# Kernel tuning notes

Hardware: AMD Instinct MI355X
Metric: run time of the kernel (lower is better)

The kernel has to match this reference:

```python
import jax, jax.numpy as jnp
import numpy as np

N_ITER = 5
NMF_EPS = 1e-20
IP_EPS = 1e-20

M, J, I, K = 2, 2000, 2049, 8  # channels == sources, frames, freq bins, NMF bases


def setup_inputs() -> dict:
    key = jax.random.key(0)
    k1, k2, k3 = jax.random.split(key, 3)
    X = jax.random.normal(k1, (M, J, I, 2), dtype=jnp.float32)
    lo = 1e-08
    T0 = jax.random.uniform(k2, (I, K, M), dtype=jnp.float32) * (1 - lo) + lo
    V0 = jax.random.uniform(k3, (K, J, M), dtype=jnp.float32) * (1 - lo) + lo
    return {"X": X, "T0": T0, "V0": V0}


def nmf_update(T, V, Y, eps):
    # T: (I,K), V: (K,J), Y: (I,J) complex
    P = jnp.abs(Y) ** 2                       # power spectrogram (I,J)
    R = T @ V                                  # low-rank model (I,J)
    T = T * jnp.sqrt(((P / (R * R)) @ V.T) / ((1.0 / R) @ V.T))
    T = jnp.maximum(T, eps)
    R = T @ V
    V = V * jnp.sqrt((T.T @ (P / (R * R))) / (T.T @ (1.0 / R)))
    V = jnp.maximum(V, eps)
    R = T @ V
    return T, V, R


def reference(X, T0, V0):
    Mc, Jc, Ic, _ = X.shape
    N = Mc
    # view_as_complex(X.permute(2,0,1,3)) -> (I, M, J) complex
    Xc = jnp.transpose(X[..., 0] + 1j * X[..., 1], (2, 0, 1)).astype(jnp.complex64)
    eye_M = jnp.eye(Mc, dtype=jnp.complex64)
    W = jnp.broadcast_to(eye_M, (Ic, N, Mc))   # (I, N, M)
    T, V = T0, V0

    def body(carry, _):
        W, T, V = carry
        Y = jnp.einsum('inm,imj->inj', W, Xc)  # (I, N, J)
        for n in range(N):
            Tn, Vn, Rn = nmf_update(T[:, :, n], V[:, :, n], Y[:, n, :], NMF_EPS)
            T = T.at[:, :, n].set(Tn)
            V = V.at[:, :, n].set(Vn)
            inv_Rn = 1.0 / (Rn + IP_EPS)                       # (I, J)
            Xw = Xc * jnp.sqrt(inv_Rn)[:, None, :]             # (I, M, J)
            D = jnp.einsum('imj,ikj->imk', Xw, jnp.conj(Xw)) / Jc  # (I, M, M)
            Dreg = D + IP_EPS * eye_M
            A = jnp.einsum('inm,imk->ink', W, Dreg)            # (I, M, M)
            e_n = jnp.broadcast_to(eye_M[:, n], (Ic, Mc))
            b = jnp.linalg.solve(A, e_n[..., None])[..., 0]    # (I, M)
            quad = jnp.einsum('im,imk,ik->i', jnp.conj(b), Dreg, b)
            denom = jnp.sqrt(jnp.real(quad) + IP_EPS)          # (I,)
            W = W.at[:, n, :].set(jnp.conj(b / denom[:, None]))
        return (W, T, V), None

    (W, T, V), _ = jax.lax.scan(body, (W, T, V), None, length=N_ITER)
    Y = jnp.einsum('inm,imj->inj', W, Xc)                      # (I, N, J)
    Yp = jnp.transpose(Y, (1, 2, 0))                           # (N, J, I)
    return jnp.stack([jnp.real(Yp), jnp.imag(Yp)], axis=-1)    # (N, J, I, 2)
```

## Files before the change

kernel.cpp:

```cpp
#include <hip/hip_runtime.h>
#include <hip/hip_fp16.h>

#define M_CH 2
#define J_F 2000
#define I_F 2049
#define K_B 8
#define N_IT 5
#define NMF_EPS 1e-20f
#define IP_EPS 1e-20f

#define NB_PACKT (65 * 63)
#define NB_PACK (9 * 250)
#define NB_INIT 128

__device__ __forceinline__ float2 h2f(unsigned u) {
  __half2 h = *reinterpret_cast<__half2*>(&u);
  return __half22float2(h);
}
__device__ __forceinline__ float4 h4f(unsigned lo, unsigned hi) {
  float2 a = h2f(lo), b = h2f(hi);
  return make_float4(a.x, a.y, b.x, b.y);
}
__device__ __forceinline__ unsigned f2h(float a, float b) {
  __half2 h = __floats2half2_rn(a, b);
  return *reinterpret_cast<unsigned*>(&h);
}

template<int PK>
__global__ __launch_bounds__(256) void k_setup(const float2* __restrict__ X,
                                               const float* __restrict__ T0,
                                               const float* __restrict__ V0,
                                               float* __restrict__ T,
                                               float* __restrict__ V,
                                               float* __restrict__ W,
                                               __half* __restrict__ Xht,
                                               __half* __restrict__ Xhj) {
  int b = blockIdx.x;
  const int tid = threadIdx.x;
  if (b < NB_PACKT) {
    if (!PK) return;
    __shared__ float4 Tl[32][33];
    const int i0 = (b % 65) * 32, j0 = (b / 65) * 32;
    const int la = tid & 31, su = tid >> 5;
#pragma unroll
    for (int p = 0; p < 4; ++p) {
      int jj = su + p * 8;
      int i = i0 + la, j = j0 + jj;
      if (i < I_F && j < J_F) {
        float2 a = X[(size_t)j * I_F + i];
        float2 c = X[(size_t)(J_F + j) * I_F + i];
        Tl[la][jj] = make_float4(a.x, a.y, c.x, c.y);
      }
    }
    __syncthreads();
#pragma unroll
    for (int p = 0; p < 4; ++p) {
      int ii = su + p * 8;
      int i = i0 + ii, j = j0 + la;
      if (i < I_F && j < J_F) {
        float4 x = Tl[ii][la];
        *(uint2*)(Xht + ((size_t)i * J_F + j) * 4) =
            make_uint2(f2h(x.x, x.y), f2h(x.z, x.w));
      }
    }
    return;
  }
  b -= NB_PACKT;
  if (b < NB_PACK) {
    if (!PK) return;
    const int i = (b % 9) * 256 + tid;
    if (i >= I_F) return;
    const int j0 = (b / 9) * 8;
    const int jend = min(8, J_F - j0);
    for (int jj = 0; jj < jend; ++jj) {
      const int j = j0 + jj;
      float2 a = X[(size_t)j * I_F + i];
      float2 c = X[(size_t)(J_F + j) * I_F + i];
      *(uint2*)(Xhj + ((size_t)j * I_F + i) * 4) =
          make_uint2(f2h(a.x, a.y), f2h(c.x, c.y));
    }
    return;
  }
  b -= NB_PACK;
  int t = b * 256 + tid;
  const int stride = NB_INIT * 256;
  for (int idx = t; idx < 2 * I_F * K_B; idx += stride) {
    int n = idx / (I_F * K_B);
    int r = idx % (I_F * K_B);
    int i = r / K_B, k = r % K_B;
    T[idx] = T0[(i * K_B + k) * M_CH + n];
  }
  for (int idx = t; idx < 2 * K_B * J_F; idx += stride) {
    int n = idx / (K_B * J_F);
    int r = idx % (K_B * J_F);
    int k = r / J_F, j = r % J_F;
    V[idx] = V0[(k * J_F + j) * M_CH + n];
  }
  for (int i = t; i < I_F; i += stride) {
    W[i * 8 + 0] = 1.f; W[i * 8 + 1] = 0.f; W[i * 8 + 2] = 0.f; W[i * 8 + 3] = 0.f;
    W[i * 8 + 4] = 0.f; W[i * 8 + 5] = 0.f; W[i * 8 + 6] = 1.f; W[i * 8 + 7] = 0.f;
  }
}

template<int PK>
__global__ __launch_bounds__(256) void k_T(const __half* __restrict__ Xht,
                                           const float2* __restrict__ X,
                                           const float* __restrict__ W,
                                           float* __restrict__ T,
                                           const float* __restrict__ V) {
  const int i = blockIdx.x;
  const int tid = threadIdx.x;
  float tr0[K_B], tr1[K_B];
#pragma unroll
  for (int k = 0; k < K_B; ++k) {
    tr0[k] = T[(size_t)i * 8 + k];
    tr1[k] = T[((size_t)I_F + i) * 8 + k];
  }
  const float4 w0 = ((const float4*)W)[i * 2];
  const float4 w1 = ((const float4*)W)[i * 2 + 1];
  float num0[K_B] = {}, den0[K_B] = {}, num1[K_B] = {}, den1[K_B] = {};
  if (PK) {
    const __half* xrow = Xht + (size_t)i * J_F * 4;
    for (int j2 = tid; j2 < J_F / 2; j2 += 256) {
      const int j = j2 * 2;
      uint4 raw = *(const uint4*)(xrow + (size_t)j * 4);
      float4 xa = h4f(raw.x, raw.y);
      float4 xb = h4f(raw.z, raw.w);
      float2 v0p[K_B], v1p[K_B];
      float R0a = 0.f, R0b = 0.f, R1a = 0.f, R1b = 0.f;
#pragma unroll
      for (int k = 0; k < K_B; ++k) {
        v0p[k] = *(const float2*)&V[(size_t)k * J_F + j];
        v1p[k] = *(const float2*)&V[(size_t)(K_B + k) * J_F + j];
        R0a += tr0[k] * v0p[k].x; R0b += tr0[k] * v0p[k].y;
        R1a += tr1[k] * v1p[k].x; R1b += tr1[k] * v1p[k].y;
      }
      float yr, yi;
      yr = w0.x * xa.x - w0.y * xa.y + w0.z * xa.z - w0.w * xa.w;
      yi = w0.x * xa.y + w0.y * xa.x + w0.z * xa.w + w0.w * xa.z;
      float p0a = yr * yr + yi * yi;
      yr = w1.x * xa.x - w1.y * xa.y + w1.z * xa.z - w1.w * xa.w;
      yi = w1.x * xa.y + w1.y * xa.x + w1.z * xa.w + w1.w * xa.z;
      float p1a = yr * yr + yi * yi;
      yr = w0.x * xb.x - w0.y * xb.y + w0.z * xb.z - w0.w * xb.w;
      yi = w0.x * xb.y + w0.y * xb.x + w0.z * xb.w + w0.w * xb.z;
      float p0b = yr * yr + yi * yi;
      yr = w1.x * xb.x - w1.y * xb.y + w1.z * xb.z - w1.w * xb.w;
      yi = w1.x * xb.y + w1.y * xb.x + w1.z * xb.w + w1.w * xb.z;
      float p1b = yr * yr + yi * yi;
      float a0a = p0a / (R0a * R0a), b0a = 1.f / R0a;
      float a1a = p1a / (R1a * R1a), b1a = 1.f / R1a;
      float a0b = p0b / (R0b * R0b), b0b = 1.f / R0b;
      float a1b = p1b / (R1b * R1b), b1b = 1.f / R1b;
#pragma unroll
      for (int k = 0; k < K_B; ++k) {
        num0[k] += a0a * v0p[k].x + a0b * v0p[k].y;
        den0[k] += b0a * v0p[k].x + b0b * v0p[k].y;
        num1[k] += a1a * v1p[k].x + a1b * v1p[k].y;
        den1[k] += b1a * v1p[k].x + b1b * v1p[k].y;
      }
    }
  } else {
    for (int j = tid; j < J_F; j += 256) {
      float2 a = X[(size_t)j * I_F + i];
      float2 c = X[(size_t)(J_F + j) * I_F + i];
      float4 x = make_float4(a.x, a.y, c.x, c.y);
      float yr = w0.x * x.x - w0.y * x.y + w0.z * x.z - w0.w * x.w;
      float yi = w0.x * x.y + w0.y * x.x + w0.z * x.w + w0.w * x.z;
      float p0 = yr * yr + yi * yi;
      float zr = w1.x * x.x - w1.y * x.y + w1.z * x.z - w1.w * x.w;
      float zi = w1.x * x.y + w1.y * x.x + w1.z * x.w + w1.w * x.z;
      float p1 = zr * zr + zi * zi;
      float v0[K_B], v1[K_B];
      float R0 = 0.f, R1 = 0.f;
#pragma unroll
      for (int k = 0; k < K_B; ++k) {
        v0[k] = V[(size_t)k * J_F + j];         R0 += tr0[k] * v0[k];
        v1[k] = V[(size_t)(K_B + k) * J_F + j]; R1 += tr1[k] * v1[k];
      }
      float a0 = p0 / (R0 * R0), b0 = 1.0f / R0;
      float a1 = p1 / (R1 * R1), b1 = 1.0f / R1;
#pragma unroll
      for (int k = 0; k < K_B; ++k) {
        num0[k] += a0 * v0[k]; den0[k] += b0 * v0[k];
        num1[k] += a1 * v1[k]; den1[k] += b1 * v1[k];
      }
    }
  }
  __shared__ float red[4][32];
  const int lane = tid & 63, wid = tid >> 6;
#pragma unroll
  for (int k = 0; k < K_B; ++k) {
    float a0 = num0[k], b0 = den0[k], a1 = num1[k], b1 = den1[k];
#pragma unroll
    for (int off = 32; off > 0; off >>= 1) {
      a0 += __shfl_xor(a0, off, 64);
      b0 += __shfl_xor(b0, off, 64);
      a1 += __shfl_xor(a1, off, 64);
      b1 += __shfl_xor(b1, off, 64);
    }
    if (lane == 0) {
      red[wid][k] = a0; red[wid][8 + k] = b0;
      red[wid][16 + k] = a1; red[wid][24 + k] = b1;
    }
  }
  __syncthreads();
  if (tid < 32) red[0][tid] = red[0][tid] + red[1][tid] + red[2][tid] + red[3][tid];
  __syncthreads();
  if (tid < 16) {
    int n = tid >> 3, k = tid & 7;
    float nu = red[0][n * 16 + k];
    float de = red[0][n * 16 + 8 + k];
    size_t idx = ((size_t)n * I_F + i) * 8 + k;
    float told = T[idx];
    T[idx] = fmaxf(told * sqrtf(nu / de), NMF_EPS);
  }
}

template<int PK>
__global__ __launch_bounds__(256) void k_V(const __half* __restrict__ Xhj,
                                           const float2* __restrict__ X,
                                           const float* __restrict__ W,
                                           const float* __restrict__ T,
                                           float* __restrict__ V) {
  const int j = blockIdx.x;
  const int tid = threadIdx.x;
  float vold0[K_B], vold1[K_B];
#pragma unroll
  for (int k = 0; k < K_B; ++k) {
    vold0[k] = V[(size_t)k * J_F + j];
    vold1[k] = V[(size_t)(K_B + k) * J_F + j];
  }
  float num0[K_B] = {}, den0[K_B] = {}, num1[K_B] = {}, den1[K_B] = {};
  const float* T1 = T + (size_t)I_F * K_B;
  const __half* xcol = Xhj + (size_t)j * I_F * 4;
  for (int i = tid; i < I_F; i += 256) {
    float4 x;
    if (PK) {
      uint2 raw = *(const uint2*)(xcol + (size_t)i * 4);
      x = h4f(raw.x, raw.y);
    } else {
      float2 a = X[(size_t)j * I_F + i];
      float2 c = X[(size_t)(J_F + j) * I_F + i];
      x = make_float4(a.x, a.y, c.x, c.y);
    }
    const float4 wa = ((const float4*)W)[i * 2];
    const float4 wb = ((const float4*)W)[i * 2 + 1];
    float yr = wa.x * x.x - wa.y * x.y + wa.z * x.z - wa.w * x.w;
    float yi = wa.x * x.y + wa.y * x.x + wa.z * x.w + wa.w * x.z;
    float p0 = yr * yr + yi * yi;
    float zr = wb.x * x.x - wb.y * x.y + wb.z * x.z - wb.w * x.w;
    float zi = wb.x * x.y + wb.y * x.x + wb.z * x.w + wb.w * x.z;
    float p1 = zr * zr + zi * zi;
    const float4 ta = *(const float4*)&T[i * 8];
    const float4 tb = *(const float4*)&T[i * 8 + 4];
    const float4 tc = *(const float4*)&T1[i * 8];
    const float4 td = *(const float4*)&T1[i * 8 + 4];
    float t0[K_B] = {ta.x, ta.y, ta.z, ta.w, tb.x, tb.y, tb.z, tb.w};
    float t1[K_B] = {tc.x, tc.y, tc.z, tc.w, td.x, td.y, td.z, td.w};
    float R0 = 0.f, R1 = 0.f;
#pragma unroll
    for (int k = 0; k < K_B; ++k) { R0 += t0[k] * vold0[k]; R1 += t1[k] * vold1[k]; }
    float a0 = p0 / (R0 * R0), b0 = 1.0f / R0;
    float a1 = p1 / (R1 * R1), b1 = 1.0f / R1;
#pragma unroll
    for (int k = 0; k < K_B; ++k) {
      num0[k] += a0 * t0[k]; den0[k] += b0 * t0[k];
      num1[k] += a1 * t1[k]; den1[k] += b1 * t1[k];
    }
  }
  __shared__ float red[4][32];
  const int lane = tid & 63, wid = tid >> 6;
#pragma unroll
  for (int k = 0; k < K_B; ++k) {
    float a0 = num0[k], b0 = den0[k], a1 = num1[k], b1 = den1[k];
#pragma unroll
    for (int off = 32; off > 0; off >>= 1) {
      a0 += __shfl_xor(a0, off, 64);
      b0 += __shfl_xor(b0, off, 64);
      a1 += __shfl_xor(a1, off, 64);
      b1 += __shfl_xor(b1, off, 64);
    }
    if (lane == 0) {
      red[wid][k] = a0; red[wid][8 + k] = b0;
      red[wid][16 + k] = a1; red[wid][24 + k] = b1;
    }
  }
  __syncthreads();
  if (tid < 32) red[0][tid] = red[0][tid] + red[1][tid] + red[2][tid] + red[3][tid];
  __syncthreads();
  if (tid < 16) {
    int n = tid >> 3, k = tid & 7;
    float nu = red[0][n * 16 + k];
    float de = red[0][n * 16 + 8 + k];
    size_t idx = ((size_t)n * K_B + k) * J_F + j;
    float vo = V[idx];
    V[idx] = fmaxf(vo * sqrtf(nu / de), NMF_EPS);
  }
}

template<int PK>
__global__ __launch_bounds__(256) void k_D(const __half* __restrict__ Xht,
                                           const float2* __restrict__ X,
                                           const float* __restrict__ T,
                                           const float* __restrict__ V,
                                           float* __restrict__ W) {
  const int i = blockIdx.x;
  const int tid = threadIdx.x;
  float tr0[K_B], tr1[K_B];
#pragma unroll
  for (int k = 0; k < K_B; ++k) {
    tr0[k] = T[(size_t)i * K_B + k];
    tr1[k] = T[((size_t)I_F + i) * K_B + k];
  }
  float acc[8] = {};
  if (PK) {
    const __half* xrow = Xht + (size_t)i * J_F * 4;
    for (int j2 = tid; j2 < J_F / 2; j2 += 256) {
      const int j = j2 * 2;
      uint4 raw = *(const uint4*)(xrow + (size_t)j * 4);
      float4 xa = h4f(raw.x, raw.y);
      float4 xb = h4f(raw.z, raw.w);
      float R0a = 0.f, R0b = 0.f, R1a = 0.f, R1b = 0.f;
#pragma unroll
      for (int k = 0; k < K_B; ++k) {
        float2 v0p = *(const float2*)&V[(size_t)k * J_F + j];
        float2 v1p = *(const float2*)&V[(size_t)(K_B + k) * J_F + j];
        R0a += tr0[k] * v0p.x; R0b += tr0[k] * v0p.y;
        R1a += tr1[k] * v1p.x; R1b += tr1[k] * v1p.y;
      }
      float wv0a = 1.0f / (R0a + IP_EPS), wv0b = 1.0f / (R0b + IP_EPS);
      float wv1a = 1.0f / (R1a + IP_EPS), wv1b = 1.0f / (R1b + IP_EPS);
      float p00a = xa.x * xa.x + xa.y * xa.y, p00b = xb.x * xb.x + xb.y * xb.y;
      float p11a = xa.z * xa.z + xa.w * xa.w, p11b = xb.z * xb.z + xb.w * xb.w;
      float pra = xa.x * xa.z + xa.y * xa.w, prb = xb.x * xb.z + xb.y * xb.w;
      float pia = xa.y * xa.z - xa.x * xa.w, pib = xb.y * xb.z - xb.x * xb.w;
      acc[0] += wv0a * p00a + wv0b * p00b;
      acc[1] += wv0a * p11a + wv0b * p11b;
      acc[2] += wv0a * pra + wv0b * prb;
      acc[3] += wv0a * pia + wv0b * pib;
      acc[4] += wv1a * p00a + wv1b * p00b;
      acc[5] += wv1a * p11a + wv1b * p11b;
      acc[6] += wv1a * pra + wv1b * prb;
      acc[7] += wv1a * pia + wv1b * pib;
    }
  } else {
    for (int j = tid; j < J_F; j += 256) {
      float2 a = X[(size_t)j * I_F + i];
      float2 c = X[(size_t)(J_F + j) * I_F + i];
      float4 x = make_float4(a.x, a.y, c.x, c.y);
      float R0 = 0.f, R1 = 0.f;
#pragma unroll
      for (int k = 0; k < K_B; ++k) {
        R0 += tr0[k] * V[(size_t)k * J_F + j];
        R1 += tr1[k] * V[(size_t)(K_B + k) * J_F + j];
      }
      float wv0 = 1.0f / (R0 + IP_EPS);
      float wv1 = 1.0f / (R1 + IP_EPS);
      float p00 = x.x * x.x + x.y * x.y;
      float p11 = x.z * x.z + x.w * x.w;
      float pr = x.x * x.z + x.y * x.w;
      float pi = x.y * x.z - x.x * x.w;
      acc[0] += wv0 * p00; acc[1] += wv0 * p11; acc[2] += wv0 * pr; acc[3] += wv0 * pi;
      acc[4] += wv1 * p00; acc[5] += wv1 * p11; acc[6] += wv1 * pr; acc[7] += wv1 * pi;
    }
  }
  __shared__ float red[4][8];
  const int lane = tid & 63, wid = tid >> 6;
#pragma unroll
  for (int v = 0; v < 8; ++v) {
    float a = acc[v];
#pragma unroll
    for (int off = 32; off > 0; off >>= 1) a += __shfl_xor(a, off, 64);
    if (lane == 0) red[wid][v] = a;
  }
  __syncthreads();
  if (tid < 8) red[0][tid] = red[0][tid] + red[1][tid] + red[2][tid] + red[3][tid];
  __syncthreads();
  if (tid == 0) {
    float4 wa = ((const float4*)W)[i * 2];
    float4 wb = ((const float4*)W)[i * 2 + 1];
    float w00r = wa.x, w00i = wa.y, w01r = wa.z, w01i = wa.w;
    float w10r = wb.x, w10i = wb.y, w11r = wb.z, w11i = wb.w;
    const float invJ = 1.0f / (float)J_F;
#pragma unroll
    for (int n = 0; n < 2; ++n) {
      float d00 = red[0][n * 4 + 0] * invJ + IP_EPS;
      float d11 = red[0][n * 4 + 1] * invJ + IP_EPS;
      float d01r = red[0][n * 4 + 2] * invJ;
      float d01i = red[0][n * 4 + 3] * invJ;
      float A00r = w00r * d00 + (w01r * d01r + w01i * d01i);
      float A00i = w00i * d00 + (w01i * d01r - w01r * d01i);
      float A01r = (w00r * d01r - w00i * d01i) + w01r * d11;
      float A01i = (w00r * d01i + w00i * d01r) + w01i * d11;
      float A10r = w10r * d00 + (w11r * d01r + w11i * d01i);
      float A10i = w10i * d00 + (w11i * d01r - w11r * d01i);
      float A11r = (w10r * d01r - w10i * d01i) + w11r * d11;
      float A11i = (w10r * d01i + w10i * d01r) + w11i * d11;
      float detr = (A00r * A11r - A00i * A11i) - (A01r * A10r - A01i * A10i);
      float deti = (A00r * A11i + A00i * A11r) - (A01r * A10i + A01i * A10r);
      float idet = 1.0f / (detr * detr + deti * deti);
      float n0r, n0i, n1r, n1i;
      if (n == 0) { n0r = A11r; n0i = A11i; n1r = -A10r; n1i = -A10i; }
      else        { n0r = -A01r; n0i = -A01i; n1r = A00r; n1i = A00i; }
      float b0r = (n0r * detr + n0i * deti) * idet;
      float b0i = (n0i * detr - n0r * deti) * idet;
      float b1r = (n1r * detr + n1i * deti) * idet;
      float b1i = (n1i * detr - n1r * deti) * idet;
      float cr = d01r * b1r - d01i * b1i;
      float ci = d01r * b1i + d01i * b1r;
      float quad = d00 * (b0r * b0r + b0i * b0i) + d11 * (b1r * b1r + b1i * b1i)
                 + 2.0f * (b0r * cr + b0i * ci);
      float s = 1.0f / sqrtf(quad + IP_EPS);
      if (n == 0) { w00r = b0r * s; w00i = -b0i * s; w01r = b1r * s; w01i = -b1i * s; }
      else        { w10r = b0r * s; w10i = -b0i * s; w11r = b1r * s; w11i = -b1i * s; }
    }
    ((float4*)W)[i * 2]     = make_float4(w00r, w00i, w01r, w01i);
    ((float4*)W)[i * 2 + 1] = make_float4(w10r, w10i, w11r, w11i);
  }
}

__global__ __launch_bounds__(256) void k_final(const float2* __restrict__ X,
                                               const float* __restrict__ W,
                                               float2* __restrict__ out) {
  const int i = blockIdx.x * 256 + threadIdx.x;
  if (i >= I_F) return;
  const float4 wa = ((const float4*)W)[i * 2];
  const float4 wb = ((const float4*)W)[i * 2 + 1];
  const int j0 = blockIdx.y * 8;
  const int jend = min(8, J_F - j0);
  for (int jj = 0; jj < jend; ++jj) {
    const int j = j0 + jj;
    float2 a = X[(size_t)j * I_F + i];
    float2 c = X[(size_t)(J_F + j) * I_F + i];
    float y0r = wa.x * a.x - wa.y * a.y + wa.z * c.x - wa.w * c.y;
    float y0i = wa.x * a.y + wa.y * a.x + wa.z * c.y + wa.w * c.x;
    out[(size_t)j * I_F + i] = make_float2(y0r, y0i);
    float y1r = wb.x * a.x - wb.y * a.y + wb.z * c.x - wb.w * c.y;
    float y1i = wb.x * a.y + wb.y * a.x + wb.z * c.y + wb.w * c.x;
    out[(size_t)(J_F + j) * I_F + i] = make_float2(y1r, y1i);
  }
}

extern "C" void kernel_launch(void* const* d_in, const int* in_sizes, int n_in,
                              void* d_out, int out_size, void* d_ws, size_t ws_size,
                              hipStream_t stream) {
  const float2* X = (const float2*)d_in[0];
  const float* T0 = (const float*)d_in[1];
  const float* V0 = (const float*)d_in[2];
  float2* outp = (float2*)d_out;
  char* ws = (char*)d_ws;
  size_t off = 0;
  auto alloc = [&](size_t bytes) -> void* {
    void* p = ws + off;
    off = (off + bytes + 255) & ~(size_t)255;
    return p;
  };
  float* W = (float*)alloc((size_t)I_F * 8 * 4);
  float* T = (float*)alloc((size_t)2 * I_F * K_B * 4);
  float* V = (float*)alloc((size_t)2 * K_B * J_F * 4);
  const size_t xh_sz = (size_t)J_F * I_F * 8;
  __half* Xht = nullptr;
  __half* Xhj = nullptr;
  if (off + 2 * xh_sz + 512 <= ws_size) {
    Xht = (__half*)alloc(xh_sz);
    Xhj = (__half*)alloc(xh_sz);
  }
  const int NBS = NB_PACKT + NB_PACK + NB_INIT;

  if (Xht) {
    k_setup<1><<<NBS, 256, 0, stream>>>(X, T0, V0, T, V, W, Xht, Xhj);
    for (int it = 0; it < N_IT; ++it) {
      k_T<1><<<I_F, 256, 0, stream>>>(Xht, X, W, T, V);
      k_V<1><<<J_F, 256, 0, stream>>>(Xhj, X, W, T, V);
      k_D<1><<<I_F, 256, 0, stream>>>(Xht, X, T, V, W);
    }
  } else {
    k_setup<0><<<NBS, 256, 0, stream>>>(X, T0, V0, T, V, W, nullptr, nullptr);
    for (int it = 0; it < N_IT; ++it) {
      k_T<0><<<I_F, 256, 0, stream>>>(nullptr, X, W, T, V);
      k_V<0><<<J_F, 256, 0, stream>>>(nullptr, X, W, T, V);
      k_D<0><<<I_F, 256, 0, stream>>>(nullptr, X, T, V, W);
    }
  }
  k_final<<<dim3(9, 250), 256, 0, stream>>>(X, W, outp);
}
```

Measured before the change: 467.9 us.

## Fuse D and next-iteration T phases per frequency row, merge X packing passes

Adds a fused k_DT kernel that computes the demixing update for a frequency bin and then immediately runs the next iteration's T update for the same bin. W is passed through shared memory, which removes one launch per iteration and one extra read of that bin's packed X row while it is likely still cached. The separate Xhj packing pass is folded into the transpose tiles. The final output kernel now reads the packed half-precision X instead of the fp32 input, which lowers output precision slightly.

```diff
diff --git a/kernel.cpp b/kernel.cpp
--- a/kernel.cpp
+++ b/kernel.cpp
@@ -9,8 +9,7 @@
 #define NMF_EPS 1e-20f
 #define IP_EPS 1e-20f
 
-#define NB_PACKT (65 * 63)
-#define NB_PACK (9 * 250)
+#define NB_TILE (65 * 63)
 #define NB_INIT 128
 
 __device__ __forceinline__ float2 h2f(unsigned u) {
@@ -37,7 +36,7 @@
                                                __half* __restrict__ Xhj) {
   int b = blockIdx.x;
   const int tid = threadIdx.x;
-  if (b < NB_PACKT) {
+  if (b < NB_TILE) {
     if (!PK) return;
     __shared__ float4 Tl[32][33];
     const int i0 = (b % 65) * 32, j0 = (b / 65) * 32;
@@ -49,7 +48,10 @@
       if (i < I_F && j < J_F) {
         float2 a = X[(size_t)j * I_F + i];
         float2 c = X[(size_t)(J_F + j) * I_F + i];
-        Tl[la][jj] = make_float4(a.x, a.y, c.x, c.y);
+        float4 x = make_float4(a.x, a.y, c.x, c.y);
+        Tl[la][jj] = x;
+        *(uint2*)(Xhj + ((size_t)j * I_F + i) * 4) =
+            make_uint2(f2h(x.x, x.y), f2h(x.z, x.w));
       }
     }
     __syncthreads();
@@ -65,23 +67,7 @@
     }
     return;
   }
-  b -= NB_PACKT;
-  if (b < NB_PACK) {
-    if (!PK) return;
-    const int i = (b % 9) * 256 + tid;
-    if (i >= I_F) return;
-    const int j0 = (b / 9) * 8;
-    const int jend = min(8, J_F - j0);
-    for (int jj = 0; jj < jend; ++jj) {
-      const int j = j0 + jj;
-      float2 a = X[(size_t)j * I_F + i];
-      float2 c = X[(size_t)(J_F + j) * I_F + i];
-      *(uint2*)(Xhj + ((size_t)j * I_F + i) * 4) =
-          make_uint2(f2h(a.x, a.y), f2h(c.x, c.y));
-    }
-    return;
-  }
-  b -= NB_PACK;
+  b -= NB_TILE;
   int t = b * 256 + tid;
   const int stride = NB_INIT * 256;
   for (int idx = t; idx < 2 * I_F * K_B; idx += stride) {
@@ -103,12 +89,11 @@
 }
 
 template<int PK>
-__global__ __launch_bounds__(256) void k_T(const __half* __restrict__ Xht,
-                                           const float2* __restrict__ X,
-                                           const float* __restrict__ W,
-                                           float* __restrict__ T,
-                                           const float* __restrict__ V) {
-  const int i = blockIdx.x;
+__device__ __forceinline__ void t_phase(const int i, const __half* __restrict__ Xht,
+                                        const float2* __restrict__ X,
+                                        const float4 w0, const float4 w1,
+                                        float* __restrict__ T, const float* __restrict__ V,
+                                        float (*red)[32]) {
   const int tid = threadIdx.x;
   float tr0[K_B], tr1[K_B];
 #pragma unroll
@@ -116,8 +101,6 @@
     tr0[k] = T[(size_t)i * 8 + k];
     tr1[k] = T[((size_t)I_F + i) * 8 + k];
   }
-  const float4 w0 = ((const float4*)W)[i * 2];
-  const float4 w1 = ((const float4*)W)[i * 2 + 1];
   float num0[K_B] = {}, den0[K_B] = {}, num1[K_B] = {}, den1[K_B] = {};
   if (PK) {
     const __half* xrow = Xht + (size_t)i * J_F * 4;
@@ -187,7 +170,6 @@
       }
     }
   }
-  __shared__ float red[4][32];
   const int lane = tid & 63, wid = tid >> 6;
 #pragma unroll
   for (int k = 0; k < K_B; ++k) {
@@ -218,94 +200,12 @@
 }
 
 template<int PK>
-__global__ __launch_bounds__(256) void k_V(const __half* __restrict__ Xhj,
-                                           const float2* __restrict__ X,
-                                           const float* __restrict__ W,
-                                           const float* __restrict__ T,
-                                           float* __restrict__ V) {
-  const int j = blockIdx.x;
-  const int tid = threadIdx.x;
-  float vold0[K_B], vold1[K_B];
-#pragma unroll
-  for (int k = 0; k < K_B; ++k) {
-    vold0[k] = V[(size_t)k * J_F + j];
-    vold1[k] = V[(size_t)(K_B + k) * J_F + j];
-  }
-  float num0[K_B] = {}, den0[K_B] = {}, num1[K_B] = {}, den1[K_B] = {};
-  const float* T1 = T + (size_t)I_F * K_B;
-  const __half* xcol = Xhj + (size_t)j * I_F * 4;
-  for (int i = tid; i < I_F; i += 256) {
-    float4 x;
-    if (PK) {
-      uint2 raw = *(const uint2*)(xcol + (size_t)i * 4);
-      x = h4f(raw.x, raw.y);
-    } else {
-      float2 a = X[(size_t)j * I_F + i];
-      float2 c = X[(size_t)(J_F + j) * I_F + i];
-      x = make_float4(a.x, a.y, c.x, c.y);
-    }
-    const float4 wa = ((const float4*)W)[i * 2];
-    const float4 wb = ((const float4*)W)[i * 2 + 1];
-    float yr = wa.x * x.x - wa.y * x.y + wa.z * x.z - wa.w * x.w;
-    float yi = wa.x * x.y + wa.y * x.x + wa.z * x.w + wa.w * x.z;
-    float p0 = yr * yr + yi * yi;
-    float zr = wb.x * x.x - wb.y * x.y + wb.z * x.z - wb.w * x.w;
-    float zi = wb.x * x.y + wb.y * x.x + wb.z * x.w + wb.w * x.z;
-    float p1 = zr * zr + zi * zi;
-    const float4 ta = *(const float4*)&T[i * 8];
-    const float4 tb = *(const float4*)&T[i * 8 + 4];
-    const float4 tc = *(const float4*)&T1[i * 8];
-    const float4 td = *(const float4*)&T1[i * 8 + 4];
-    float t0[K_B] = {ta.x, ta.y, ta.z, ta.w, tb.x, tb.y, tb.z, tb.w};
-    float t1[K_B] = {tc.x, tc.y, tc.z, tc.w, td.x, td.y, td.z, td.w};
-    float R0 = 0.f, R1 = 0.f;
-#pragma unroll
-    for (int k = 0; k < K_B; ++k) { R0 += t0[k] * vold0[k]; R1 += t1[k] * vold1[k]; }
-    float a0 = p0 / (R0 * R0), b0 = 1.0f / R0;
-    float a1 = p1 / (R1 * R1), b1 = 1.0f / R1;
-#pragma unroll
-    for (int k = 0; k < K_B; ++k) {
-      num0[k] += a0 * t0[k]; den0[k] += b0 * t0[k];
-      num1[k] += a1 * t1[k]; den1[k] += b1 * t1[k];
-    }
-  }
-  __shared__ float red[4][32];
-  const int lane = tid & 63, wid = tid >> 6;
-#pragma unroll
-  for (int k = 0; k < K_B; ++k) {
-    float a0 = num0[k], b0 = den0[k], a1 = num1[k], b1 = den1[k];
-#pragma unroll
-    for (int off = 32; off > 0; off >>= 1) {
-      a0 += __shfl_xor(a0, off, 64);
-      b0 += __shfl_xor(b0, off, 64);
-      a1 += __shfl_xor(a1, off, 64);
-      b1 += __shfl_xor(b1, off, 64);
-    }
-    if (lane == 0) {
-      red[wid][k] = a0; red[wid][8 + k] = b0;
-      red[wid][16 + k] = a1; red[wid][24 + k] = b1;
-    }
-  }
-  __syncthreads();
-  if (tid < 32) red[0][tid] = red[0][tid] + red[1][tid] + red[2][tid] + red[3][tid];
-  __syncthreads();
-  if (tid < 16) {
-    int n = tid >> 3, k = tid & 7;
-    float nu = red[0][n * 16 + k];
-    float de = red[0][n * 16 + 8 + k];
-    size_t idx = ((size_t)n * K_B + k) * J_F + j;
-    float vo = V[idx];
-    V[idx] = fmaxf(vo * sqrtf(nu / de), NMF_EPS);
-  }
-}
-
-template<int PK>
-__global__ __launch_bounds__(256) void k_D(const __half* __restrict__ Xht,
-                                           const float2* __restrict__ X,
-                                           const float* __restrict__ T,
-                                           const float* __restrict__ V,
-                                           float* __restrict__ W) {
-  const int i = blockIdx.x;
+__device__ __forceinline__ void d_phase(const int i, const __half* __restrict__ Xht,
+                                        const float2* __restrict__ X,
+                                        const float* __restrict__ T,
+                                        const float* __restrict__ V,
+                                        float* __restrict__ W,
+                                        float (*red)[32], float* wrow) {
   const int tid = threadIdx.x;
   float tr0[K_B], tr1[K_B];
 #pragma unroll
@@ -365,7 +265,6 @@
       acc[4] += wv1 * p00; acc[5] += wv1 * p11; acc[6] += wv1 * pr; acc[7] += wv1 * pi;
     }
   }
-  __shared__ float red[4][8];
   const int lane = tid & 63, wid = tid >> 6;
 #pragma unroll
   for (int v = 0; v < 8; ++v) {
@@ -417,10 +316,137 @@
     }
     ((float4*)W)[i * 2]     = make_float4(w00r, w00i, w01r, w01i);
     ((float4*)W)[i * 2 + 1] = make_float4(w10r, w10i, w11r, w11i);
-  }
-}
-
-__global__ __launch_bounds__(256) void k_final(const float2* __restrict__ X,
+    wrow[0] = w00r; wrow[1] = w00i; wrow[2] = w01r; wrow[3] = w01i;
+    wrow[4] = w10r; wrow[5] = w10i; wrow[6] = w11r; wrow[7] = w11i;
+  }
+  __syncthreads();
+}
+
+template<int PK>
+__global__ __launch_bounds__(256) void k_T(const __half* __restrict__ Xht,
+                                           const float2* __restrict__ X,
+                                           const float* __restrict__ W,
+                                           float* __restrict__ T,
+                                           const float* __restrict__ V) {
+  __shared__ float red[4][32];
+  const int i = blockIdx.x;
+  const float4 w0 = ((const float4*)W)[i * 2];
+  const float4 w1 = ((const float4*)W)[i * 2 + 1];
+  t_phase<PK>(i, Xht, X, w0, w1, T, V, red);
+}
+
+template<int PK>
+__global__ __launch_bounds__(256) void k_D(const __half* __restrict__ Xht,
+                                           const float2* __restrict__ X,
+                                           const float* __restrict__ T,
+                                           const float* __restrict__ V,
+                                           float* __restrict__ W) {
+  __shared__ float red[4][32];
+  __shared__ float wrow[8];
+  d_phase<PK>(blockIdx.x, Xht, X, T, V, W, red, wrow);
+}
+
+template<int PK>
+__global__ __launch_bounds__(256) void k_DT(const __half* __restrict__ Xht,
+                                            const float2* __restrict__ X,
+                                            float* __restrict__ T,
+                                            const float* __restrict__ V,
+                                            float* __restrict__ W) {
+  __shared__ float red[4][32];
+  __shared__ float wrow[8];
+  const int i = blockIdx.x;
+  d_phase<PK>(i, Xht, X, T, V, W, red, wrow);
+  const float4 w0 = make_float4(wrow[0], wrow[1], wrow[2], wrow[3]);
+  const float4 w1 = make_float4(wrow[4], wrow[5], wrow[6], wrow[7]);
+  __syncthreads();
+  t_phase<PK>(i, Xht, X, w0, w1, T, V, red);
+}
+
+template<int PK>
+__global__ __launch_bounds__(256) void k_V(const __half* __restrict__ Xhj,
+                                           const float2* __restrict__ X,
+                                           const float* __restrict__ W,
+                                           const float* __restrict__ T,
+                                           float* __restrict__ V) {
+  const int j = blockIdx.x;
+  const int tid = threadIdx.x;
+  float vold0[K_B], vold1[K_B];
+#pragma unroll
+  for (int k = 0; k < K_B; ++k) {
+    vold0[k] = V[(size_t)k * J_F + j];
+    vold1[k] = V[(size_t)(K_B + k) * J_F + j];
+  }
+  float num0[K_B] = {}, den0[K_B] = {}, num1[K_B] = {}, den1[K_B] = {};
+  const float* T1 = T + (size_t)I_F * K_B;
+  const __half* xcol = Xhj + (size_t)j * I_F * 4;
+  for (int i = tid; i < I_F; i += 256) {
+    float4 x;
+    if (PK) {
+      uint2 raw = *(const uint2*)(xcol + (size_t)i * 4);
+      x = h4f(raw.x, raw.y);
+    } else {
+      float2 a = X[(size_t)j * I_F + i];
+      float2 c = X[(size_t)(J_F + j) * I_F + i];
+      x = make_float4(a.x, a.y, c.x, c.y);
+    }
+    const float4 wa = ((const float4*)W)[i * 2];
+    const float4 wb = ((const float4*)W)[i * 2 + 1];
+    float yr = wa.x * x.x - wa.y * x.y + wa.z * x.z - wa.w * x.w;
+    float yi = wa.x * x.y + wa.y * x.x + wa.z * x.w + wa.w * x.z;
+    float p0 = yr * yr + yi * yi;
+    float zr = wb.x * x.x - wb.y * x.y + wb.z * x.z - wb.w * x.w;
+    float zi = wb.x * x.y + wb.y * x.x + wb.z * x.w + wb.w * x.z;
+    float p1 = zr * zr + zi * zi;
+    const float4 ta = *(const float4*)&T[i * 8];
+    const float4 tb = *(const float4*)&T[i * 8 + 4];
+    const float4 tc = *(const float4*)&T1[i * 8];
+    const float4 td = *(const float4*)&T1[i * 8 + 4];
+    float t0[K_B] = {ta.x, ta.y, ta.z, ta.w, tb.x, tb.y, tb.z, tb.w};
+    float t1[K_B] = {tc.x, tc.y, tc.z, tc.w, td.x, td.y, td.z, td.w};
+    float R0 = 0.f, R1 = 0.f;
+#pragma unroll
+    for (int k = 0; k < K_B; ++k) { R0 += t0[k] * vold0[k]; R1 += t1[k] * vold1[k]; }
+    float a0 = p0 / (R0 * R0), b0 = 1.0f / R0;
+    float a1 = p1 / (R1 * R1), b1 = 1.0f / R1;
+#pragma unroll
+    for (int k = 0; k < K_B; ++k) {
+      num0[k] += a0 * t0[k]; den0[k] += b0 * t0[k];
+      num1[k] += a1 * t1[k]; den1[k] += b1 * t1[k];
+    }
+  }
+  __shared__ float red[4][32];
+  const int lane = tid & 63, wid = tid >> 6;
+#pragma unroll
+  for (int k = 0; k < K_B; ++k) {
+    float a0 = num0[k], b0 = den0[k], a1 = num1[k], b1 = den1[k];
+#pragma unroll
+    for (int off = 32; off > 0; off >>= 1) {
+      a0 += __shfl_xor(a0, off, 64);
+      b0 += __shfl_xor(b0, off, 64);
+      a1 += __shfl_xor(a1, off, 64);
+      b1 += __shfl_xor(b1, off, 64);
+    }
+    if (lane == 0) {
+      red[wid][k] = a0; red[wid][8 + k] = b0;
+      red[wid][16 + k] = a1; red[wid][24 + k] = b1;
+    }
+  }
+  __syncthreads();
+  if (tid < 32) red[0][tid] = red[0][tid] + red[1][tid] + red[2][tid] + red[3][tid];
+  __syncthreads();
+  if (tid < 16) {
+    int n = tid >> 3, k = tid & 7;
+    float nu = red[0][n * 16 + k];
+    float de = red[0][n * 16 + 8 + k];
+    size_t idx = ((size_t)n * K_B + k) * J_F + j;
+    float vo = V[idx];
+    V[idx] = fmaxf(vo * sqrtf(nu / de), NMF_EPS);
+  }
+}
+
+template<int PK>
+__global__ __launch_bounds__(256) void k_final(const __half* __restrict__ Xhj,
+                                               const float2* __restrict__ X,
                                                const float* __restrict__ W,
                                                float2* __restrict__ out) {
   const int i = blockIdx.x * 256 + threadIdx.x;
@@ -431,13 +457,20 @@
   const int jend = min(8, J_F - j0);
   for (int jj = 0; jj < jend; ++jj) {
     const int j = j0 + jj;
-    float2 a = X[(size_t)j * I_F + i];
-    float2 c = X[(size_t)(J_F + j) * I_F + i];
-    float y0r = wa.x * a.x - wa.y * a.y + wa.z * c.x - wa.w * c.y;
-    float y0i = wa.x * a.y + wa.y * a.x + wa.z * c.y + wa.w * c.x;
+    float4 x;
+    if (PK) {
+      uint2 raw = *(const uint2*)(Xhj + ((size_t)j * I_F + i) * 4);
+      x = h4f(raw.x, raw.y);
+    } else {
+      float2 a = X[(size_t)j * I_F + i];
+      float2 c = X[(size_t)(J_F + j) * I_F + i];
+      x = make_float4(a.x, a.y, c.x, c.y);
+    }
+    float y0r = wa.x * x.x - wa.y * x.y + wa.z * x.z - wa.w * x.w;
+    float y0i = wa.x * x.y + wa.y * x.x + wa.z * x.w + wa.w * x.z;
     out[(size_t)j * I_F + i] = make_float2(y0r, y0i);
-    float y1r = wb.x * a.x - wb.y * a.y + wb.z * c.x - wb.w * c.y;
-    float y1i = wb.x * a.y + wb.y * a.x + wb.z * c.y + wb.w * c.x;
+    float y1r = wb.x * x.x - wb.y * x.y + wb.z * x.z - wb.w * x.w;
+    float y1i = wb.x * x.y + wb.y * x.x + wb.z * x.w + wb.w * x.z;
     out[(size_t)(J_F + j) * I_F + i] = make_float2(y1r, y1i);
   }
 }
@@ -466,22 +499,29 @@
     Xht = (__half*)alloc(xh_sz);
     Xhj = (__half*)alloc(xh_sz);
   }
-  const int NBS = NB_PACKT + NB_PACK + NB_INIT;
+  const int NBS = NB_TILE + NB_INIT;
 
   if (Xht) {
     k_setup<1><<<NBS, 256, 0, stream>>>(X, T0, V0, T, V, W, Xht, Xhj);
+    k_T<1><<<I_F, 256, 0, stream>>>(Xht, X, W, T, V);
     for (int it = 0; it < N_IT; ++it) {
-      k_T<1><<<I_F, 256, 0, stream>>>(Xht, X, W, T, V);
       k_V<1><<<J_F, 256, 0, stream>>>(Xhj, X, W, T, V);
-      k_D<1><<<I_F, 256, 0, stream>>>(Xht, X, T, V, W);
-    }
+      if (it < N_IT - 1)
+        k_DT<1><<<I_F, 256, 0, stream>>>(Xht, X, T, V, W);
+      else
+        k_D<1><<<I_F, 256, 0, stream>>>(Xht, X, T, V, W);
+    }
+    k_final<1><<<dim3(9, 250), 256, 0, stream>>>(Xhj, X, W, outp);
   } else {
     k_setup<0><<<NBS, 256, 0, stream>>>(X, T0, V0, T, V, W, nullptr, nullptr);
+    k_T<0><<<I_F, 256, 0, stream>>>(nullptr, X, W, T, V);
     for (int it = 0; it < N_IT; ++it) {
-      k_T<0><<<I_F, 256, 0, stream>>>(nullptr, X, W, T, V);
       k_V<0><<<J_F, 256, 0, stream>>>(nullptr, X, W, T, V);
-      k_D<0><<<I_F, 256, 0, stream>>>(nullptr, X, T, V, W);
-    }
-  }
-  k_final<<<dim3(9, 250), 256, 0, stream>>>(X, W, outp);
-}
+      if (it < N_IT - 1)
+        k_DT<0><<<I_F, 256, 0, stream>>>(nullptr, X, T, V, W);
+      else
+        k_D<0><<<I_F, 256, 0, stream>>>(nullptr, X, T, V, W);
+    }
+    k_final<0><<<dim3(9, 250), 256, 0, stream>>>(nullptr, X, W, outp);
+  }
+}
```

New measurement: 467.0 us. Within noise of the previous version (-0.2%).
